# Performance work log

Measured on AMD Instinct MI355X. Metric: run time of the kernel, lower is better.

Reference implementation:

```python
import jax, jax.numpy as jnp
import numpy as np

T, N, H, DIN = 128, 256, 512, 255  # inputs last dim = DIN + 1 (trailing action channel)
PACK = H + 5  # packed state: a(1), loc(1), scale(1), v(1), h(H), p(1)


def setup_inputs() -> dict:
    key = jax.random.key(0)
    ks = jax.random.split(key, 12)
    f32 = jnp.float32
    def rn(k, shape, scale):
        return jax.random.normal(k, shape, dtype=f32) * scale
    si, sh = 1.0 / np.sqrt(DIN), 1.0 / np.sqrt(H)
    return {
        "inputs": jax.random.normal(ks[0], (T, N, DIN + 1), dtype=f32),
        "hx": rn(ks[1], (1, N, PACK), 0.1),
        "eps": jax.random.normal(ks[2], (T, N, 1), dtype=f32),
        "Wih": rn(ks[3], (3 * H, DIN), si),
        "Whh": rn(ks[4], (3 * H, H), sh),
        "bih": jnp.zeros((3 * H,), f32),
        "bhh": jnp.zeros((3 * H,), f32),
        "Wa0": rn(ks[5], (H, H), sh), "ba0": jnp.zeros((H,), f32),
        "Wa1": rn(ks[6], (H, H), sh), "ba1": jnp.zeros((H,), f32),
        "Wloc": rn(ks[7], (1, H), sh), "bloc": jnp.zeros((1,), f32),
        "logstd": jnp.zeros((1,), f32),
        "Wc0": rn(ks[8], (H, H), sh), "bc0": jnp.zeros((H,), f32),
        "Wc1": rn(ks[9], (H, H), sh), "bc1": jnp.zeros((H,), f32),
        "Wv": rn(ks[10], (1, H), sh), "bv": jnp.zeros((1,), f32),
    }


def _forward(inputs, hx, eps, Wih, Whh, bih, bhh, Wa0, ba0, Wa1, ba1,
             Wloc, bloc, logstd, Wc0, bc0, Wc1, bc1, Wv, bv):
    inputs = jax.lax.stop_gradient(inputs)  # module calls inputs.detach()
    obs, actions = inputs[..., :DIN], inputs[..., DIN:]
    hx0 = hx[0]                       # [N, PACK] after squeeze_(0)
    h0 = hx0[:, 4:4 + H]              # initial GRU hidden state
    p = hx0[:, H + 4:H + 5]           # [N,1], passed through unchanged

    def step(h, x_t):
        # PyTorch GRU cell math
        gi = x_t @ Wih.T + bih        # [N, 3H]
        gh = h @ Whh.T + bhh          # [N, 3H]
        ir, iz, in_ = jnp.split(gi, 3, axis=-1)
        hr, hz, hn = jnp.split(gh, 3, axis=-1)
        r = jax.nn.sigmoid(ir + hr)
        z = jax.nn.sigmoid(iz + hz)
        n = jnp.tanh(in_ + r * hn)
        h_new = (1.0 - z) * n + z * h
        return h_new, h_new

    _, hs = jax.lax.scan(step, h0, obs)  # [T, N, H]; hn == h for 1-layer unidir GRU

    def mlp2(x, W0, b0, W1, b1):
        return jnp.tanh(jnp.tanh(x @ W0.T + b0) @ W1.T + b1)

    # heads don't feed back into the recurrence -> apply to all timesteps at once
    loc = mlp2(hs, Wa0, ba0, Wa1, ba1) @ Wloc.T + bloc        # [T, N, 1]
    scale = jnp.broadcast_to(jnp.exp(logstd), loc.shape)      # DiagGaussian scale
    v = mlp2(hs, Wc0, bc0, Wc1, bc1) @ Wv.T + bv              # [T, N, 1]

    # sample_new: replace entries of A where actions < 0 with dist.sample()
    sample = jax.lax.stop_gradient(loc + scale * eps)         # .sample() is non-differentiable
    a = jnp.where(actions < 0, sample, actions)

    p_full = jnp.broadcast_to(p, (T, N, 1))
    # pack() order follows RecurrentState fields: a, loc, scale, v, h, p
    return jnp.concatenate([a, loc, scale, v, hs, p_full], axis=-1)  # [T, N, PACK]


def reference(inputs, hx, eps, Wih, Whh, bih, bhh, Wa0, ba0, Wa1, ba1,
              Wloc, bloc, logstd, Wc0, bc0, Wc1, bc1, Wv, bv):
    packed = _forward(inputs, hx, eps, Wih, Whh, bih, bhh, Wa0, ba0, Wa1, ba1,
                      Wloc, bloc, logstd, Wc0, bc0, Wc1, bc1, Wv, bv)
    return (packed, packed[-1:])
```

## Files before the change

kernel.cpp:

```cpp
#include <hip/hip_runtime.h>

typedef unsigned short u16;
typedef unsigned long long u64;
typedef __bf16 bf16x8 __attribute__((ext_vector_type(8)));
typedef float f32x4 __attribute__((ext_vector_type(4)));

#define T_STEPS 128
#define NB 256
#define HDIM 512
#define DIN_ 255
#define PACK_ 517
#define TN 32768

__device__ __forceinline__ float b2f(u16 u) {
    union { unsigned int i; float f; } v; v.i = ((unsigned int)u) << 16; return v.f;
}
__device__ __forceinline__ u16 f2b(float f) {
    union { float f; unsigned int i; } v; v.f = f;
    unsigned int r = v.i + 0x7FFFu + ((v.i >> 16) & 1u);
    return (u16)(r >> 16);
}
__device__ __forceinline__ float sigm(float x) { return 1.f / (1.f + __expf(-x)); }
__device__ __forceinline__ float ftanh(float x) { return 2.f * sigm(2.f * x) - 1.f; }

__device__ __forceinline__ bf16x8 ldx4(const u16* p) {
    f32x4 t;
    asm volatile("global_load_dwordx4 %0, %1, off" : "=v"(t) : "v"(p) : "memory");
    union { f32x4 f; bf16x8 b; } u; u.f = t; return u.b;
}
#define WAIT_VMCNT(N) asm volatile("s_waitcnt vmcnt(" #N ")" ::: "memory")
#define WAIT_LGKM0    asm volatile("s_waitcnt lgkmcnt(0)" ::: "memory")

template<int DO_TANH, int K, int MT>
__global__ __launch_bounds__(256) void gemm_bt(const u16* __restrict__ A,
                                               const u16* __restrict__ B,
                                               const float* __restrict__ bias,
                                               u16* __restrict__ C, int N) {
    __shared__ u16 lds[64 * K];
    int n0 = blockIdx.x * 64;
    int w = threadIdx.x >> 6, l = threadIdx.x & 63;
    int la = l & 15, lb = l >> 4;
    for (int idx = threadIdx.x; idx < 8 * K; idx += 256) {
        int kq = idx >> 6, row = idx & 63;
        *(bf16x8*)(lds + (size_t)idx * 8) =
            *(const bf16x8*)(B + (size_t)(n0 + row) * K + kq * 8);
    }
    __syncthreads();
    const u16* bq[4];
    #pragma unroll
    for (int c = 0; c < 4; ++c) bq[c] = lds + ((size_t)lb * 64 + 16 * c + la) * 8;

    for (int mt = 0; mt < MT; ++mt) {
        int m0 = (blockIdx.y * MT + mt) * 64;
        int mw = m0 + 16 * w;
        const u16* Ap = A + (size_t)(mw + la) * K + 8 * lb;
        f32x4 acc[4] = {};
        #pragma unroll
        for (int k0 = 0; k0 < K; k0 += 32) {
            bf16x8 a = *(const bf16x8*)(Ap + k0);
            #pragma unroll
            for (int c = 0; c < 4; ++c)
                acc[c] = __builtin_amdgcn_mfma_f32_16x16x32_bf16(
                    a, *(const bf16x8*)(bq[c] + (size_t)k0 * 64), acc[c], 0, 0, 0);
        }
        #pragma unroll
        for (int c = 0; c < 4; ++c) {
            int n = n0 + 16 * c + la;
            float bv = bias[n];
            #pragma unroll
            for (int r = 0; r < 4; ++r) {
                int m = mw + 4 * lb + r;
                float v = acc[c][r] + bv;
                if (DO_TANH) v = ftanh(v);
                C[(size_t)m * N + n] = f2b(v);
            }
        }
    }
}

__global__ __launch_bounds__(256, 1) void gru_persist(
    const u16* __restrict__ h0b, const float* __restrict__ hx,
    const u16* __restrict__ whh_b, const float* __restrict__ bhh,
    const u16* __restrict__ gi_b,
    u16* __restrict__ hs_b, unsigned int* __restrict__ bar) {
    extern __shared__ u16 lds[];
    __shared__ unsigned s_locv;
    const int tid = threadIdx.x;
    const int bid = blockIdx.x;
    const int g = bid & 7, s = bid >> 3;
    const int ks = s * 32, m0 = g * 32;
    const int w = tid >> 6, l = tid & 63;
    const int la = l & 15, lb = l >> 4;
    const int rw = w >> 1, cw = w & 1;
    const int mw = m0 + 16 * rw;
    const int kc = ks + 16 * cw;

    unsigned myx;
    asm volatile("s_getreg_b32 %0, hwreg(HW_REG_XCC_ID)" : "=s"(myx));
    myx = (myx & 15u) + 1u;
    unsigned int* tbl = bar + 512;
    if (tid == 0)
        __hip_atomic_fetch_add(tbl + bid, myx, __ATOMIC_RELAXED,
                               __HIP_MEMORY_SCOPE_AGENT);

    for (int idx = tid; idx < 6144; idx += 256) {
        int kq = idx / 96, row = idx - kq * 96;
        int gg = row >> 5, rr = row & 31;
        *(bf16x8*)(lds + (size_t)idx * 8) =
            *(const bf16x8*)(whh_b + (size_t)(gg * HDIM + ks + rr) * HDIM + kq * 8);
    }
    const u16* bq[3];
    #pragma unroll
    for (int c = 0; c < 3; ++c)
        bq[c] = lds + (size_t)(lb * 96 + c * 32 + 16 * cw + la) * 8;
    float bh[3];
    #pragma unroll
    for (int gg = 0; gg < 3; ++gg) bh[gg] = bhh[gg * HDIM + kc + la];
    float hp[4];
    #pragma unroll
    for (int r = 0; r < 4; ++r)
        hp[r] = hx[(size_t)(mw + 4 * lb + r) * PACK_ + 4 + kc + la];

    if (tid == 0) {
        unsigned vals[16];
        int guard = 0;
        bool ok;
        do {
            ok = true;
            #pragma unroll
            for (int k = 0; k < 16; ++k) {
                vals[k] = __hip_atomic_fetch_add(tbl + g + 8 * k, 0u,
                                                 __ATOMIC_RELAXED,
                                                 __HIP_MEMORY_SCOPE_AGENT);
                ok = ok && (vals[k] != 0u);
            }
            if (!ok) __builtin_amdgcn_s_sleep(8);
        } while (!ok && ++guard < (1 << 16));
        unsigned lv = ok ? 1u : 0u;
        #pragma unroll
        for (int k = 1; k < 16; ++k) lv &= (unsigned)(vals[k] == vals[0]);
        s_locv = lv;
    }
    u16* packbuf = lds + 49152 + w * 256;
    __syncthreads();
    const bool loc = (s_locv != 0);
    unsigned int* mybar = bar + g * 64;

    for (int t = 0; t < T_STEPS; ++t) {
        const u16* gi_t = gi_b + (size_t)t * NB * 3 * HDIM;

        u16 giv[3][4];
        #pragma unroll
        for (int r = 0; r < 4; ++r) {
            const u16* gp = gi_t + (size_t)(mw + 4 * lb + r) * 1536 + kc + la;
            #pragma unroll
            for (int gg = 0; gg < 3; ++gg) giv[gg][r] = gp[gg * HDIM];
        }

        if (t > 0) {
            unsigned tgt = 16u * (unsigned)t;
            int guard = 0;
            for (;;) {
                unsigned v = 0;
                if (l == 0) {
                    if (loc)
                        asm volatile(
                            "global_atomic_add %0, %1, %2, off sc0\n\t"
                            "s_waitcnt vmcnt(0)"
                            : "=v"(v) : "v"(mybar), "v"(0u) : "memory");
                    else
                        v = __hip_atomic_fetch_add(mybar, 0u, __ATOMIC_RELAXED,
                                                   __HIP_MEMORY_SCOPE_AGENT);
                }
                v = (unsigned)__builtin_amdgcn_readfirstlane((int)v);
                if (v >= tgt || ++guard > (1 << 20)) break;
                __builtin_amdgcn_s_sleep(1);
            }
            asm volatile("" ::: "memory");
        }

        const u16* Ap = (t ? hs_b + (size_t)(t - 1) * NB * HDIM : h0b)
                        + (size_t)(mw + la) * HDIM + 8 * lb;
        bf16x8 a[16];
        #pragma unroll
        for (int kk = 0; kk < 16; ++kk) a[kk] = ldx4(Ap + 32 * kk);

        f32x4 acc[3] = {};
        WAIT_VMCNT(8);
        __builtin_amdgcn_sched_barrier(0);
        #pragma unroll
        for (int kk = 0; kk < 8; ++kk) {
            #pragma unroll
            for (int c = 0; c < 3; ++c)
                acc[c] = __builtin_amdgcn_mfma_f32_16x16x32_bf16(
                    a[kk], *(const bf16x8*)(bq[c] + (size_t)kk * 3072), acc[c], 0, 0, 0);
        }
        WAIT_VMCNT(0);
        __builtin_amdgcn_sched_barrier(0);
        #pragma unroll
        for (int kk = 8; kk < 16; ++kk) {
            #pragma unroll
            for (int c = 0; c < 3; ++c)
                acc[c] = __builtin_amdgcn_mfma_f32_16x16x32_bf16(
                    a[kk], *(const bf16x8*)(bq[c] + (size_t)kk * 3072), acc[c], 0, 0, 0);
        }

        float hnewv[4];
        #pragma unroll
        for (int r = 0; r < 4; ++r) {
            float rr2 = sigm(b2f(giv[0][r]) + acc[0][r] + bh[0]);
            float zz  = sigm(b2f(giv[1][r]) + acc[1][r] + bh[1]);
            float nn  = ftanh(b2f(giv[2][r]) + rr2 * (acc[2][r] + bh[2]));
            float hnew = (1.f - zz) * nn + zz * hp[r];
            hp[r] = hnew;
            hnewv[r] = hnew;
        }

        #pragma unroll
        for (int r = 0; r < 4; ++r) {
            float nbv = __shfl_xor(hnewv[r], 1, 64);
            if (!(la & 1)) {
                unsigned pk = (unsigned)f2b(hnewv[r]) | ((unsigned)f2b(nbv) << 16);
                *(unsigned*)(packbuf + (4 * lb + r) * 16 + la) = pk;
            }
        }
        WAIT_LGKM0;
        __builtin_amdgcn_sched_barrier(0);
        u16* hs_t = hs_b + (size_t)t * NB * HDIM;
        if (l < 32) {
            bf16x8 hv = *(const bf16x8*)(packbuf + (l >> 1) * 16 + 8 * (l & 1));
            union { bf16x8 b; f32x4 f; } u; u.b = hv;
            u16* sp = hs_t + (size_t)(mw + (l >> 1)) * HDIM + kc + 8 * (l & 1);
            if (loc) asm volatile("global_store_dwordx4 %0, %1, off"
                                  :: "v"(sp), "v"(u.f) : "memory");
            else     asm volatile("global_store_dwordx4 %0, %1, off sc0 sc1"
                                  :: "v"(sp), "v"(u.f) : "memory");
        }
        WAIT_VMCNT(0);
        __syncthreads();
        if (t < T_STEPS - 1 && tid == 0) {
            if (loc)
                asm volatile("global_atomic_add %0, %1, off"
                             :: "v"(mybar), "v"(1u) : "memory");
            else
                __hip_atomic_fetch_add(mybar, 1u, __ATOMIC_RELAXED,
                                       __HIP_MEMORY_SCOPE_AGENT);
        }
    }
}

__global__ void expand_h(const u16* __restrict__ hs, float* __restrict__ out) {
    int idx = blockIdx.x * 256 + threadIdx.x;
    if (idx >= TN * 256) return;
    int m = idx >> 8, kk = (idx & 255) * 2;
    unsigned pk = *(const unsigned*)(hs + (size_t)m * HDIM + kk);
    float* o = out + (size_t)m * PACK_ + 4 + kk;
    o[0] = b2f((u16)(pk & 0xFFFFu));
    o[1] = b2f((u16)(pk >> 16));
}

__global__ __launch_bounds__(256) void head_dot(const u16* __restrict__ X,
                                                const u16* __restrict__ W,
                                                const float* __restrict__ b,
                                                float* __restrict__ out, int off) {
    int wid = (int)((blockIdx.x * blockDim.x + threadIdx.x) >> 6);
    int l = threadIdx.x & 63;
    if (wid >= TN) return;
    bf16x8 xv = *(const bf16x8*)(X + (size_t)wid * HDIM + 8 * l);
    bf16x8 wv = *(const bf16x8*)(W + 8 * l);
    float s = 0.f;
    #pragma unroll
    for (int j = 0; j < 8; ++j) s += (float)xv[j] * (float)wv[j];
    #pragma unroll
    for (int d = 32; d; d >>= 1) s += __shfl_down(s, d, 64);
    if (l == 0) out[(size_t)wid * PACK_ + off] = s + b[0];
}

__global__ void prep_w(const float* __restrict__ Wih, const float* __restrict__ Whh,
                       const float* __restrict__ Wa0, const float* __restrict__ Wa1,
                       const float* __restrict__ Wloc, const float* __restrict__ Wc0,
                       const float* __restrict__ Wc1, const float* __restrict__ Wv,
                       const float* __restrict__ hx,
                       u16* Wih_b, u16* Whh_b, u16* Wa0_b, u16* Wa1_b,
                       u16* Wloc_b, u16* Wc0_b, u16* Wc1_b, u16* Wv_b,
                       float* h0f, u16* h0b) {
    int i = blockIdx.x * 256 + threadIdx.x;
    if (i < 1536 * 256) { int r = i >> 8, c = i & 255;
        Wih_b[i] = (c < DIN_) ? f2b(Wih[r * DIN_ + c]) : (u16)0; return; }
    i -= 1536 * 256;
    if (i < 1536 * 512) { Whh_b[i] = f2b(Whh[i]); return; } i -= 1536 * 512;
    if (i < 512 * 512) { Wa0_b[i] = f2b(Wa0[i]); return; } i -= 512 * 512;
    if (i < 512 * 512) { Wa1_b[i] = f2b(Wa1[i]); return; } i -= 512 * 512;
    if (i < 512 * 512) { Wc0_b[i] = f2b(Wc0[i]); return; } i -= 512 * 512;
    if (i < 512 * 512) { Wc1_b[i] = f2b(Wc1[i]); return; } i -= 512 * 512;
    if (i < 512) { Wloc_b[i] = f2b(Wloc[i]); return; } i -= 512;
    if (i < 512) { Wv_b[i] = f2b(Wv[i]); return; } i -= 512;
    if (i < NB * HDIM) { int n = i >> 9, k = i & 511;
        float v = hx[n * PACK_ + 4 + k]; h0f[i] = v; h0b[i] = f2b(v); return; }
}

__global__ void prep_obs(const float* __restrict__ in, u16* __restrict__ obs) {
    int idx = blockIdx.x * 256 + threadIdx.x;
    if (idx >= TN * 32) return;
    int m = idx >> 5, j = idx & 31;
    const float* src = in + (size_t)m * 256 + 8 * j;
    union { u16 s[8]; uint4 u; } t;
    #pragma unroll
    for (int q = 0; q < 8; ++q) t.s[q] = f2b(src[q]);
    if (j == 31) t.s[7] = 0;
    *(uint4*)(obs + (size_t)m * 256 + 8 * j) = t.u;
}

__global__ void finalize_out(const float* __restrict__ in, const float* __restrict__ eps,
                             const float* __restrict__ hx, const float* __restrict__ logstd,
                             float* __restrict__ out) {
    int m = blockIdx.x * 256 + threadIdx.x;
    if (m >= TN) return;
    int n = m & (NB - 1);
    float scale = __expf(logstd[0]);
    float loc = out[(size_t)m * PACK_ + 1];
    float act = in[(size_t)m * 256 + DIN_];
    float a = (act < 0.f) ? (loc + scale * eps[m]) : act;
    out[(size_t)m * PACK_ + 0] = a;
    out[(size_t)m * PACK_ + 2] = scale;
    out[(size_t)m * PACK_ + PACK_ - 1] = hx[n * PACK_ + PACK_ - 1];
}

__global__ void tail_copy(float* __restrict__ out) {
    int i = blockIdx.x * 256 + threadIdx.x;
    if (i >= NB * PACK_) return;
    out[(size_t)T_STEPS * NB * PACK_ + i] = out[(size_t)(T_STEPS - 1) * NB * PACK_ + i];
}

extern "C" void kernel_launch(void* const* d_in, const int* in_sizes, int n_in,
                              void* d_out, int out_size, void* d_ws, size_t ws_size,
                              hipStream_t stream) {
    const float* inputs = (const float*)d_in[0];
    const float* hx     = (const float*)d_in[1];
    const float* eps    = (const float*)d_in[2];
    const float* Wih    = (const float*)d_in[3];
    const float* Whh    = (const float*)d_in[4];
    const float* bih    = (const float*)d_in[5];
    const float* bhh    = (const float*)d_in[6];
    const float* Wa0    = (const float*)d_in[7];
    const float* ba0    = (const float*)d_in[8];
    const float* Wa1    = (const float*)d_in[9];
    const float* ba1    = (const float*)d_in[10];
    const float* Wloc   = (const float*)d_in[11];
    const float* bloc   = (const float*)d_in[12];
    const float* logstd = (const float*)d_in[13];
    const float* Wc0    = (const float*)d_in[14];
    const float* bc0    = (const float*)d_in[15];
    const float* Wc1    = (const float*)d_in[16];
    const float* bc1    = (const float*)d_in[17];
    const float* Wv     = (const float*)d_in[18];
    const float* bv     = (const float*)d_in[19];
    float* out = (float*)d_out;
    char* ws = (char*)d_ws;

    const size_t o_gi   = 0;
    const size_t o_buf0 = 0;
    const size_t o_buf1 = 33554432;
    const size_t o_hs   = 100663296;
    const size_t o_obs  = o_hs + 33554432;
    const size_t o_whh  = o_obs + 16777216;
    const size_t o_wih  = o_whh + 1572864;
    const size_t o_wa0  = o_wih + 786432;
    const size_t o_wa1  = o_wa0 + 524288;
    const size_t o_wc0  = o_wa1 + 524288;
    const size_t o_wc1  = o_wc0 + 524288;
    const size_t o_wloc = o_wc1 + 524288;
    const size_t o_wv   = o_wloc + 1024;
    const size_t o_h0f  = o_wv + 1024;
    const size_t o_h0b  = o_h0f + 524288;
    const size_t o_bar  = o_h0b + 262144;
    const size_t NEED   = o_bar + 4096;
    if (ws_size < NEED) return;

    u16*   gi_b   = (u16*)(ws + o_gi);
    u16*   buf0   = (u16*)(ws + o_buf0);
    u16*   buf1   = (u16*)(ws + o_buf1);
    u16*   hs_b   = (u16*)(ws + o_hs);
    u16*   obs_b  = (u16*)(ws + o_obs);
    u16*   whh_b  = (u16*)(ws + o_whh);
    u16*   wih_b  = (u16*)(ws + o_wih);
    u16*   wa0_b  = (u16*)(ws + o_wa0);
    u16*   wa1_b  = (u16*)(ws + o_wa1);
    u16*   wc0_b  = (u16*)(ws + o_wc0);
    u16*   wc1_b  = (u16*)(ws + o_wc1);
    u16*   wloc_b = (u16*)(ws + o_wloc);
    u16*   wv_b   = (u16*)(ws + o_wv);
    float* h0f    = (float*)(ws + o_h0f);
    u16*   h0b    = (u16*)(ws + o_h0b);
    unsigned int* bar = (unsigned int*)(ws + o_bar);

    static bool attr_set = false;
    if (!attr_set) {
        hipFuncSetAttribute((const void*)gru_persist,
                            hipFuncAttributeMaxDynamicSharedMemorySize, 102400);
        attr_set = true;
    }

    hipMemsetAsync(bar, 0, 4096, stream);

    prep_w<<<9220, 256, 0, stream>>>(Wih, Whh, Wa0, Wa1, Wloc, Wc0, Wc1, Wv, hx,
                                     wih_b, whh_b, wa0_b, wa1_b, wloc_b, wc0_b, wc1_b, wv_b,
                                     h0f, h0b);
    prep_obs<<<4096, 256, 0, stream>>>(inputs, obs_b);

    gemm_bt<0, 256, 8><<<dim3(24, 64), 256, 0, stream>>>(obs_b, wih_b, bih, gi_b, 1536);

    gru_persist<<<128, 256, 102400, stream>>>(h0b, hx, whh_b, bhh, gi_b, hs_b, bar);

    expand_h<<<32768, 256, 0, stream>>>(hs_b, out);

    gemm_bt<1, 512, 8><<<dim3(8, 64), 256, 0, stream>>>(hs_b, wa0_b, ba0, buf0, 512);
    gemm_bt<1, 512, 8><<<dim3(8, 64), 256, 0, stream>>>(buf0, wa1_b, ba1, buf1, 512);
    head_dot<<<8192, 256, 0, stream>>>(buf1, wloc_b, bloc, out, 1);
    gemm_bt<1, 512, 8><<<dim3(8, 64), 256, 0, stream>>>(hs_b, wc0_b, bc0, buf0, 512);
    gemm_bt<1, 512, 8><<<dim3(8, 64), 256, 0, stream>>>(buf0, wc1_b, bc1, buf1, 512);
    head_dot<<<8192, 256, 0, stream>>>(buf1, wv_b, bv, out, 3);

    finalize_out<<<128, 256, 0, stream>>>(inputs, eps, hx, logstd, out);
    tail_copy<<<518, 256, 0, stream>>>(out);
}
```

Measured before the change: 1.569 ms.

## Replace shared group barrier counter with per-block flag lines and parallel polling

Each of the 16 blocks in a group now increments its own cache-line-separated counter instead of one shared atomic counter. Wave 0 polls all 16 flags in parallel with lanes 0-15 and uses exponential ALU-spin backoff instead of s_sleep, then a __syncthreads releases the block. The goal is to cut atomic contention on a single line in the per-timestep inter-block barrier of the persistent GRU. In exchange every block issues 16 polling atomics per probe, the barrier gains an extra workgroup sync, and the backoff can add latency once the flags are already set.

```diff
diff --git a/kernel.cpp b/kernel.cpp
--- a/kernel.cpp
+++ b/kernel.cpp
@@ -98,7 +98,7 @@
     unsigned myx;
     asm volatile("s_getreg_b32 %0, hwreg(HW_REG_XCC_ID)" : "=s"(myx));
     myx = (myx & 15u) + 1u;
-    unsigned int* tbl = bar + 512;
+    unsigned int* tbl = bar + 8192;
     if (tid == 0)
         __hip_atomic_fetch_add(tbl + bid, myx, __ATOMIC_RELAXED,
                                __HIP_MEMORY_SCOPE_AGENT);
@@ -144,7 +144,8 @@
     u16* packbuf = lds + 49152 + w * 256;
     __syncthreads();
     const bool loc = (s_locv != 0);
-    unsigned int* mybar = bar + g * 64;
+    unsigned int* myline = bar + (g * 16 + s) * 64;
+    unsigned int* pline  = bar + (g * 16 + (l & 15)) * 64;
 
     for (int t = 0; t < T_STEPS; ++t) {
         const u16* gi_t = gi_b + (size_t)t * NB * 3 * HDIM;
@@ -158,24 +159,31 @@
         }
 
         if (t > 0) {
-            unsigned tgt = 16u * (unsigned)t;
-            int guard = 0;
-            for (;;) {
-                unsigned v = 0;
-                if (l == 0) {
-                    if (loc)
-                        asm volatile(
-                            "global_atomic_add %0, %1, %2, off sc0\n\t"
-                            "s_waitcnt vmcnt(0)"
-                            : "=v"(v) : "v"(mybar), "v"(0u) : "memory");
-                    else
-                        v = __hip_atomic_fetch_add(mybar, 0u, __ATOMIC_RELAXED,
-                                                   __HIP_MEMORY_SCOPE_AGENT);
+            if (w == 0) {
+                int guard = 0, delay = 32;
+                for (;;) {
+                    bool okl = true;
+                    if (l < 16) {
+                        unsigned v;
+                        if (loc)
+                            asm volatile(
+                                "global_atomic_add %0, %1, %2, off sc0\n\t"
+                                "s_waitcnt vmcnt(0)"
+                                : "=v"(v) : "v"(pline), "v"(0u) : "memory");
+                        else
+                            v = __hip_atomic_fetch_add(pline, 0u, __ATOMIC_RELAXED,
+                                                       __HIP_MEMORY_SCOPE_AGENT);
+                        okl = ((int)v >= t);
+                    }
+                    if (__all(okl) || ++guard > (1 << 14)) break;
+                    float z = (float)delay;
+                    for (int q = 0; q < delay; ++q)
+                        z = __builtin_fmaf(z, 1.0000001f, 0.0625f);
+                    asm volatile("" :: "v"(z));
+                    delay = delay < 2048 ? delay * 2 : 2048;
                 }
-                v = (unsigned)__builtin_amdgcn_readfirstlane((int)v);
-                if (v >= tgt || ++guard > (1 << 20)) break;
-                __builtin_amdgcn_s_sleep(1);
             }
+            __syncthreads();
             asm volatile("" ::: "memory");
         }
 
@@ -241,9 +249,9 @@
         if (t < T_STEPS - 1 && tid == 0) {
             if (loc)
                 asm volatile("global_atomic_add %0, %1, off"
-                             :: "v"(mybar), "v"(1u) : "memory");
+                             :: "v"(myline), "v"(1u) : "memory");
             else
-                __hip_atomic_fetch_add(mybar, 1u, __ATOMIC_RELAXED,
+                __hip_atomic_fetch_add(myline, 1u, __ATOMIC_RELAXED,
                                        __HIP_MEMORY_SCOPE_AGENT);
         }
     }
@@ -374,7 +382,7 @@
     const size_t o_h0f  = o_wv + 1024;
     const size_t o_h0b  = o_h0f + 524288;
     const size_t o_bar  = o_h0b + 262144;
-    const size_t NEED   = o_bar + 4096;
+    const size_t NEED   = o_bar + 36864;
     if (ws_size < NEED) return;
 
     u16*   gi_b   = (u16*)(ws + o_gi);
@@ -401,7 +409,7 @@
         attr_set = true;
     }
 
-    hipMemsetAsync(bar, 0, 4096, stream);
+    hipMemsetAsync(bar, 0, 36864, stream);
 
     prep_w<<<9220, 256, 0, stream>>>(Wih, Whh, Wa0, Wa1, Wloc, Wc0, Wc1, Wv, hx,
                                      wih_b, whh_b, wa0_b, wa1_b, wloc_b, wc0_b, wc1_b, wv_b,
```

Result: faster. 1.514 ms (-3.5%).
